# Performance work log

Hardware: AMD Instinct MI355X
Metric: run time of the kernel (lower is better)

The kernel has to match this reference:

```python
import jax, jax.numpy as jnp
import numpy as np

D_MODEL = 1024
HEADS = 16
HEAD_DIM = D_MODEL // HEADS


def setup_inputs() -> dict:
    key = jax.random.key(0)
    ks = jax.random.split(key, 6)
    B, S, D = 2, 2048, D_MODEL
    scale = 1.0 / np.sqrt(D)
    x = jax.random.normal(ks[0], (B, S, D), dtype=jnp.float32)
    mask = jax.random.randint(ks[1], (B, S), 0, 2, dtype=jnp.int32)
    Wq = jax.random.normal(ks[2], (D, D), dtype=jnp.float32) * scale
    Wk = jax.random.normal(ks[3], (D, D), dtype=jnp.float32) * scale
    Wv = jax.random.normal(ks[4], (D, D), dtype=jnp.float32) * scale
    Wp = jax.random.normal(ks[5], (D, D), dtype=jnp.float32) * scale
    zb = jnp.zeros((D,), dtype=jnp.float32)
    return {"x": x, "mask": mask, "Wq": Wq, "bq": zb, "Wk": Wk, "bk": zb,
            "Wv": Wv, "bv": zb, "Wp": Wp, "bp": zb}


def reference(x, mask, Wq, bq, Wk, bk, Wv, bv, Wp, bp):
    B, S, D = x.shape
    H, Dh = HEADS, HEAD_DIM

    def split_heads(t):  # [B,S,D] -> [B,H,S,Dh]
        return t.reshape(B, S, H, Dh).transpose(0, 2, 1, 3)

    q = split_heads(x @ Wq + bq)
    k = split_heads(x @ Wk + bk)
    v = split_heads(x @ Wv + bv)

    att = jnp.einsum('bhqd,bhkd->bhqk', q, k) / jnp.sqrt(jnp.float32(Dh))
    # key-padding mask: [B,S] -> [B,1,1,S]; masked positions -> -inf
    m = (mask[:, None, None, :] != 0)
    att = jnp.where(m, att, -jnp.inf)
    att = jax.nn.softmax(att, axis=-1)
    # rows that were fully masked produce NaN -> zero them (masked_fill(isnan, 0))
    att = jnp.where(jnp.isnan(att), 0.0, att)

    y = jnp.einsum('bhqk,bhkd->bhqd', att, v)  # [B,H,S,Dh]
    y = y.transpose(0, 2, 1, 3).reshape(B, S, D)
    return y @ Wp + bp
```

## Files before the change

### kernel.cpp

```cpp
#include <hip/hip_runtime.h>
#include <math.h>

#define D_MODEL 1024
#define HEADS 16
#define HEAD_DIM 64
#define SEQ 2048
#define BATCH 2
#define KVT 64
#define QTILE 64

typedef __attribute__((ext_vector_type(8))) short bf16x8;
typedef __attribute__((ext_vector_type(4))) float f32x4;

__device__ __forceinline__ short f2bf(float f) {
    union { float f; unsigned u; } v; v.f = f;
    unsigned r = (v.u + 0x7FFFu + ((v.u >> 16) & 1u)) >> 16;
    return (short)r;
}

__device__ __forceinline__ unsigned cvt_pk_bf16(float lo, float hi) {
    unsigned r;
    asm("v_cvt_pk_bf16_f32 %0, %1, %2" : "=v"(r) : "v"(lo), "v"(hi));
    return r;
}

__global__ __launch_bounds__(256) void convert_bf16(
    const float* __restrict__ in, short* __restrict__ out, int n8) {
    int i = blockIdx.x * 256 + threadIdx.x;
    if (i >= n8) return;
    float4 a = ((const float4*)in)[2 * i];
    float4 b = ((const float4*)in)[2 * i + 1];
    short r[8] = {f2bf(a.x), f2bf(a.y), f2bf(a.z), f2bf(a.w),
                  f2bf(b.x), f2bf(b.y), f2bf(b.z), f2bf(b.w)};
    *(uint4*)(out + 8 * i) = *(uint4*)r;
}

__global__ __launch_bounds__(256) void mask_to_float(
    const int* __restrict__ mask, float* __restrict__ mf, int n) {
    int i = blockIdx.x * 256 + threadIdx.x;
    if (i < n) mf[i] = mask[i] ? 0.f : -INFINITY;
}

__global__ __launch_bounds__(256) void wtrans(
    const float* __restrict__ Wq, const float* __restrict__ Wk,
    const float* __restrict__ Wv, const float* __restrict__ Wp,
    short* __restrict__ Wqkvt, short* __restrict__ Wpt) {
    __shared__ float t[32][33];
    const int z = blockIdx.z;
    const float* W = z == 0 ? Wq : z == 1 ? Wk : z == 2 ? Wv : Wp;
    short* dst = (z < 3) ? Wqkvt + (size_t)z * 1024 * 1024 : Wpt;
    const int n0 = blockIdx.x * 32, k0 = blockIdx.y * 32;
    const int tx = threadIdx.x & 31, ty = threadIdx.x >> 5;
#pragma unroll
    for (int j = 0; j < 4; ++j)
        t[ty + j * 8][tx] = W[(size_t)(k0 + ty + j * 8) * 1024 + n0 + tx];
    __syncthreads();
#pragma unroll
    for (int j = 0; j < 4; ++j) {
        const int n = ty + j * 8;
        dst[(size_t)(n0 + n) * 1024 + k0 + tx] = f2bf(t[tx][n]);
    }
}

template <int MODE>
__global__ __launch_bounds__(256) void mfma_gemm(
    const short* __restrict__ A, const short* __restrict__ Bt,
    const float* __restrict__ b0, const float* __restrict__ b1,
    const float* __restrict__ b2, float* __restrict__ outf,
    short* __restrict__ o0, short* __restrict__ o1, short* __restrict__ o2,
    int M, int N, int K) {
    __shared__ short As[2 * 128 * 32];
    __shared__ short Bs[2 * 128 * 32];

    const int tid = threadIdx.x;
    const int wave = tid >> 6, lane = tid & 63;
    const int l15 = lane & 15, lhi = lane >> 4;
    const int wm = wave >> 1, wn = wave & 1;
    const int bm0 = blockIdx.y * 128, bn0 = blockIdx.x * 128;

    f32x4 acc[4][4];
#pragma unroll
    for (int m = 0; m < 4; ++m)
#pragma unroll
        for (int n = 0; n < 4; ++n) acc[m][n] = (f32x4){0.f, 0.f, 0.f, 0.f};

#define STAGE_G(buf, kt_)                                                         \
    {                                                                             \
        const int k0 = (kt_) * 32;                                                \
        _Pragma("unroll") for (int p = 0; p < 2; ++p) {                           \
            const int o = (wave * 2 + p) * 64 + lane;                             \
            const int r = o >> 2;                                                 \
            const int gs = (o & 3) ^ ((r >> 1) & 3);                              \
            __builtin_amdgcn_global_load_lds(                                     \
                (const __attribute__((address_space(1))) void*)(                  \
                    A + (size_t)(bm0 + r) * K + k0 + gs * 8),                     \
                (__attribute__((address_space(3))) void*)(                        \
                    As + (size_t)(buf) * 4096 + (wave * 2 + p) * 512),            \
                16, 0, 0);                                                        \
            __builtin_amdgcn_global_load_lds(                                     \
                (const __attribute__((address_space(1))) void*)(                  \
                    Bt + (size_t)(bn0 + r) * K + k0 + gs * 8),                    \
                (__attribute__((address_space(3))) void*)(                        \
                    Bs + (size_t)(buf) * 4096 + (wave * 2 + p) * 512),            \
                16, 0, 0);                                                        \
        }                                                                         \
    }

    const int NT = K / 32;
    STAGE_G(0, 0);
    __syncthreads();
    for (int kt = 0; kt < NT; ++kt) {
        const int cur = kt & 1;
        if (kt + 1 < NT) STAGE_G((kt + 1) & 1, kt + 1);
        bf16x8 af[4], bf[4];
        const int sg = (lhi ^ ((l15 >> 1) & 3)) * 16;
#pragma unroll
        for (int m = 0; m < 4; ++m)
            af[m] = *(const bf16x8*)((char*)As + cur * 8192 +
                                     (wm * 64 + m * 16 + l15) * 64 + sg);
#pragma unroll
        for (int n = 0; n < 4; ++n)
            bf[n] = *(const bf16x8*)((char*)Bs + cur * 8192 +
                                     (wn * 64 + n * 16 + l15) * 64 + sg);
        __builtin_amdgcn_s_setprio(1);
#pragma unroll
        for (int m = 0; m < 4; ++m)
#pragma unroll
            for (int n = 0; n < 4; ++n)
                acc[m][n] = __builtin_amdgcn_mfma_f32_16x16x32_bf16(af[m], bf[n], acc[m][n], 0, 0, 0);
        __builtin_amdgcn_s_setprio(0);
        __syncthreads();
    }
#undef STAGE_G

#pragma unroll
    for (int m = 0; m < 4; ++m) {
#pragma unroll
        for (int n = 0; n < 4; ++n) {
            const int col = bn0 + wn * 64 + n * 16 + l15;
#pragma unroll
            for (int rr = 0; rr < 4; ++rr) {
                const int row = bm0 + wm * 64 + m * 16 + lhi * 4 + rr;
                const float v = acc[m][n][rr];
                if (MODE == 0) {
                    outf[(size_t)row * N + col] = v + b0[col];
                } else {
                    const int which = col >> 10;
                    const int cc = col & 1023;
                    const int h = cc >> 6, dh = cc & 63;
                    const int b = row >> 11, s = row & (SEQ - 1);
                    const float bias = (which == 0 ? b0 : which == 1 ? b1 : b2)[cc];
                    short* dst = which == 0 ? o0 : which == 1 ? o1 : o2;
                    dst[(((size_t)(b * HEADS + h)) * SEQ + s) * HEAD_DIM + dh] = f2bf(v + bias);
                }
            }
        }
    }
}

__global__ __launch_bounds__(256) void transpose_v(
    const short* __restrict__ V, short* __restrict__ Vt) {
    __shared__ short t[64][66];
    const int bh = blockIdx.y, s0 = blockIdx.x * 64;
    const int tx = threadIdx.x, ty = threadIdx.y;
    const short* src = V + ((size_t)bh * SEQ + s0) * 64;
#pragma unroll
    for (int j = 0; j < 16; ++j) {
        const int sl = ty * 16 + j;
        t[sl][tx] = src[(size_t)sl * 64 + tx];
    }
    __syncthreads();
    short* dst = Vt + (size_t)bh * 64 * SEQ + s0;
#pragma unroll
    for (int j = 0; j < 16; ++j) {
        const int dh = ty * 16 + j;
        dst[(size_t)dh * SEQ + tx] = t[tx][dh];
    }
}

__global__ __launch_bounds__(256, 4) void flash_attn(
    const short* __restrict__ Q, const short* __restrict__ K,
    const short* __restrict__ Vt, const float* __restrict__ maskf,
    short* __restrict__ Y) {
    __shared__ unsigned char kt[2][KVT * 128];
    __shared__ unsigned char vt[2][HEAD_DIM * 128];
    __shared__ unsigned char pb[4][16 * 128];

    const int tid = threadIdx.x;
    const int wave = tid >> 6;
    const int lane = tid & 63;
    const int l15 = lane & 15;
    const int lhi = lane >> 4;

    const int nwg = gridDim.x;
    const int wg = blockIdx.x;
    const int swz = (wg & 7) * (nwg >> 3) + (wg >> 3);
    const int qt = swz & 31;
    const int bh = swz >> 5;
    const int b = bh >> 4;

    const int q0 = qt * QTILE + wave * 16;

    const short* Qp = Q + ((size_t)bh * SEQ + q0 + l15) * HEAD_DIM;
    bf16x8 qf[2];
    qf[0] = *(const bf16x8*)(Qp + 8 * lhi);
    qf[1] = *(const bf16x8*)(Qp + 8 * lhi + 32);

    const unsigned char* Kb8 = (const unsigned char*)(K + (size_t)bh * SEQ * HEAD_DIM);
    const unsigned char* Vb8 = (const unsigned char*)(Vt + (size_t)bh * HEAD_DIM * SEQ);
    const float* mb = maskf + b * SEQ;

#define STAGE(buf, kvi)                                                            \
    {                                                                              \
        const unsigned char* kbase = Kb8 + (size_t)(kvi) * KVT * 128;              \
        const unsigned char* vbase = Vb8 + (size_t)(kvi) * 128;                    \
        _Pragma("unroll") for (int p = 0; p < 2; ++p) {                            \
            const int o = (wave * 2 + p) * 64 + lane;                              \
            const int row = o >> 3;                                                \
            const int inner = (o & 7) * 16;                                        \
            const int src = inner ^ ((row & 7) << 4);                              \
            __builtin_amdgcn_global_load_lds(                                      \
                (const __attribute__((address_space(1))) void*)(                   \
                    kbase + row * 128 + src),                                      \
                (__attribute__((address_space(3))) void*)(                         \
                    &kt[buf][(wave * 2 + p) * 1024]),                              \
                16, 0, 0);                                                         \
            __builtin_amdgcn_global_load_lds(                                      \
                (const __attribute__((address_space(1))) void*)(                   \
                    vbase + (size_t)row * (SEQ * 2) + src),                        \
                (__attribute__((address_space(3))) void*)(                         \
                    &vt[buf][(wave * 2 + p) * 1024]),                              \
                16, 0, 0);                                                         \
        }                                                                          \
    }

    f32x4 accO[4];
    float mrow = -30000.f, lrow = 0.f;
#pragma unroll
    for (int i = 0; i < 4; ++i) accO[i] = (f32x4){0.f, 0.f, 0.f, 0.f};

    STAGE(0, 0);
    __syncthreads();

    for (int kv = 0; kv < SEQ / KVT; ++kv) {
        const int cur = kv & 1;
        if (kv + 1 < SEQ / KVT) STAGE((kv + 1) & 1, kv + 1);

        const int k0 = kv * KVT;

        f32x4 accS[4];
#pragma unroll
        for (int nt = 0; nt < 4; ++nt) accS[nt] = (f32x4){0.f, 0.f, 0.f, 0.f};
#pragma unroll
        for (int c = 0; c < 2; ++c) {
            bf16x8 kf[4];
#pragma unroll
            for (int nt = 0; nt < 4; ++nt) {
                const int key = l15 + 16 * nt;
                kf[nt] = *(const bf16x8*)(kt[cur] + key * 128 +
                                          ((16 * lhi + 64 * c) ^ ((key & 7) << 4)));
            }
            __builtin_amdgcn_s_setprio(1);
#pragma unroll
            for (int nt = 0; nt < 4; ++nt)
                accS[nt] = __builtin_amdgcn_mfma_f32_16x16x32_bf16(kf[nt], qf[c], accS[nt], 0, 0, 0);
            __builtin_amdgcn_s_setprio(0);
        }

#pragma unroll
        for (int nt = 0; nt < 4; ++nt) {
            const f32x4 ma = *(const f32x4*)(mb + k0 + 16 * nt + 4 * lhi);
#pragma unroll
            for (int r = 0; r < 4; ++r) accS[nt][r] = accS[nt][r] * 0.125f + ma[r];
        }

        float smax = accS[0][0];
#pragma unroll
        for (int nt = 0; nt < 4; ++nt)
#pragma unroll
            for (int r = 0; r < 4; ++r) smax = fmaxf(smax, accS[nt][r]);
        smax = fmaxf(smax, __shfl_xor(smax, 16));
        smax = fmaxf(smax, __shfl_xor(smax, 32));

        if (!__all(smax <= mrow + 8.f)) {
            const float mn = fmaxf(mrow, smax);
            const float alpha = __expf(mrow - mn);
            lrow *= alpha;
#pragma unroll
            for (int d = 0; d < 4; ++d)
#pragma unroll
                for (int r = 0; r < 4; ++r) accO[d][r] *= alpha;
            mrow = mn;
        }

        float rs = 0.f;
#pragma unroll
        for (int nt = 0; nt < 4; ++nt)
#pragma unroll
            for (int r = 0; r < 4; ++r) {
                const float pv = __expf(accS[nt][r] - mrow);
                accS[nt][r] = pv;
                rs += pv;
            }
        rs += __shfl_xor(rs, 16);
        rs += __shfl_xor(rs, 32);
        lrow += rs;

#pragma unroll
        for (int nt = 0; nt < 4; ++nt) {
            uint2 w;
            w.x = cvt_pk_bf16(accS[nt][0], accS[nt][1]);
            w.y = cvt_pk_bf16(accS[nt][2], accS[nt][3]);
            *(uint2*)(pb[wave] + l15 * 128 +
                      ((32 * nt + 8 * lhi) ^ ((l15 & 7) << 4))) = w;
        }

#pragma unroll
        for (int c = 0; c < 2; ++c) {
            bf16x8 pf = *(const bf16x8*)(pb[wave] + l15 * 128 +
                                         ((16 * lhi + 64 * c) ^ ((l15 & 7) << 4)));
            bf16x8 vf[4];
#pragma unroll
            for (int d = 0; d < 4; ++d) {
                const int dh = l15 + 16 * d;
                vf[d] = *(const bf16x8*)(vt[cur] + dh * 128 +
                                         ((16 * lhi + 64 * c) ^ ((dh & 7) << 4)));
            }
            __builtin_amdgcn_s_setprio(1);
#pragma unroll
            for (int d = 0; d < 4; ++d)
                accO[d] = __builtin_amdgcn_mfma_f32_16x16x32_bf16(vf[d], pf, accO[d], 0, 0, 0);
            __builtin_amdgcn_s_setprio(0);
        }
        __syncthreads();
    }
#undef STAGE

    const float inv = (lrow > 0.f) ? 1.f / lrow : 0.f;
    const int qg = q0 + l15;
    short* Yp = Y + ((size_t)b * SEQ + qg) * D_MODEL + (bh & 15) * HEAD_DIM;
#pragma unroll
    for (int d = 0; d < 4; ++d) {
        uint2 w;
        w.x = cvt_pk_bf16(accO[d][0] * inv, accO[d][1] * inv);
        w.y = cvt_pk_bf16(accO[d][2] * inv, accO[d][3] * inv);
        *(uint2*)(Yp + 16 * d + 4 * lhi) = w;
    }
}

extern "C" void kernel_launch(void* const* d_in, const int* in_sizes, int n_in,
                              void* d_out, int out_size, void* d_ws, size_t ws_size,
                              hipStream_t stream) {
    const float* x    = (const float*)d_in[0];
    const int*   mask = (const int*)  d_in[1];
    const float* Wq   = (const float*)d_in[2];
    const float* bq   = (const float*)d_in[3];
    const float* Wk   = (const float*)d_in[4];
    const float* bk   = (const float*)d_in[5];
    const float* Wv   = (const float*)d_in[6];
    const float* bv   = (const float*)d_in[7];
    const float* Wp   = (const float*)d_in[8];
    const float* bp   = (const float*)d_in[9];
    float* out = (float*)d_out;

    short* ws    = (short*)d_ws;
    short* xb    = ws;
    short* Wqkvt = xb + ((size_t)4 << 20);
    short* Wpt   = Wqkvt + ((size_t)3 << 20);
    short* Qb    = Wpt + ((size_t)1 << 20);
    short* Kb    = Qb + ((size_t)4 << 20);
    short* Vb    = Kb + ((size_t)4 << 20);
    short* Vtb   = Vb + ((size_t)4 << 20);
    short* Yb    = Vtb + ((size_t)4 << 20);
    float* maskf = (float*)Vb;

    const int M = BATCH * SEQ;

    convert_bf16<<<dim3((M * D_MODEL / 8 + 255) / 256), 256, 0, stream>>>(x, xb, M * D_MODEL / 8);
    wtrans<<<dim3(32, 32, 4), 256, 0, stream>>>(Wq, Wk, Wv, Wp, Wqkvt, Wpt);

    mfma_gemm<1><<<dim3(3 * D_MODEL / 128, M / 128), 256, 0, stream>>>(
        xb, Wqkvt, bq, bk, bv, nullptr, Qb, Kb, Vb, M, 3 * D_MODEL, D_MODEL);

    transpose_v<<<dim3(SEQ / 64, BATCH * HEADS), dim3(64, 4), 0, stream>>>(Vb, Vtb);

    mask_to_float<<<dim3((BATCH * SEQ + 255) / 256), 256, 0, stream>>>(mask, maskf, BATCH * SEQ);

    flash_attn<<<dim3(BATCH * HEADS * (SEQ / QTILE)), 256, 0, stream>>>(Qb, Kb, Vtb, maskf, Yb);

    mfma_gemm<0><<<dim3(D_MODEL / 128, M / 128), 256, 0, stream>>>(
        Yb, Wpt, bp, bp, bp, out, nullptr, nullptr, nullptr, M, D_MODEL, D_MODEL);
}
```

Baseline: 144.0 us.

## Fuse prep kernels, write V transposed from GEMM, fold softmax scale into Q

Merges the x conversion, weight transposes and mask conversion into one prep launch. The QKV GEMM epilogue now writes V directly in transposed layout with packed stores, which removes the separate transpose_v kernel and its buffer. Q is pre-scaled by log2(e)/sqrt(Dh), so attention uses the raw v_exp_f32 (exp2) and drops the per-score multiply. The rescale threshold is widened to match the base-2 domain, the P buffer swizzle changes, and P is read as two 8-byte LDS loads. The scale is applied before the bf16 rounding of Q, so numerics shift slightly.

```diff
diff --git a/kernel.cpp b/kernel.cpp
--- a/kernel.cpp
+++ b/kernel.cpp
@@ -8,6 +8,7 @@
 #define BATCH 2
 #define KVT 64
 #define QTILE 64
+#define SCALE_Q 0.18033688f
 
 typedef __attribute__((ext_vector_type(8))) short bf16x8;
 typedef __attribute__((ext_vector_type(4))) float f32x4;
@@ -24,41 +25,47 @@
     return r;
 }
 
-__global__ __launch_bounds__(256) void convert_bf16(
-    const float* __restrict__ in, short* __restrict__ out, int n8) {
-    int i = blockIdx.x * 256 + threadIdx.x;
-    if (i >= n8) return;
-    float4 a = ((const float4*)in)[2 * i];
-    float4 b = ((const float4*)in)[2 * i + 1];
-    short r[8] = {f2bf(a.x), f2bf(a.y), f2bf(a.z), f2bf(a.w),
-                  f2bf(b.x), f2bf(b.y), f2bf(b.z), f2bf(b.w)};
-    *(uint4*)(out + 8 * i) = *(uint4*)r;
-}
-
-__global__ __launch_bounds__(256) void mask_to_float(
-    const int* __restrict__ mask, float* __restrict__ mf, int n) {
-    int i = blockIdx.x * 256 + threadIdx.x;
-    if (i < n) mf[i] = mask[i] ? 0.f : -INFINITY;
-}
-
-__global__ __launch_bounds__(256) void wtrans(
-    const float* __restrict__ Wq, const float* __restrict__ Wk,
-    const float* __restrict__ Wv, const float* __restrict__ Wp,
-    short* __restrict__ Wqkvt, short* __restrict__ Wpt) {
+__device__ __forceinline__ float fexp2(float x) {
+    float r;
+    asm("v_exp_f32 %0, %1" : "=v"(r) : "v"(x));
+    return r;
+}
+
+__global__ __launch_bounds__(256) void prep(
+    const float* __restrict__ x, const float* __restrict__ Wq,
+    const float* __restrict__ Wk, const float* __restrict__ Wv,
+    const float* __restrict__ Wp, const int* __restrict__ mask,
+    short* __restrict__ xb, short* __restrict__ Wqkvt,
+    short* __restrict__ Wpt, float* __restrict__ maskf) {
     __shared__ float t[32][33];
-    const int z = blockIdx.z;
-    const float* W = z == 0 ? Wq : z == 1 ? Wk : z == 2 ? Wv : Wp;
-    short* dst = (z < 3) ? Wqkvt + (size_t)z * 1024 * 1024 : Wpt;
-    const int n0 = blockIdx.x * 32, k0 = blockIdx.y * 32;
-    const int tx = threadIdx.x & 31, ty = threadIdx.x >> 5;
-#pragma unroll
-    for (int j = 0; j < 4; ++j)
-        t[ty + j * 8][tx] = W[(size_t)(k0 + ty + j * 8) * 1024 + n0 + tx];
-    __syncthreads();
-#pragma unroll
-    for (int j = 0; j < 4; ++j) {
-        const int n = ty + j * 8;
-        dst[(size_t)(n0 + n) * 1024 + k0 + tx] = f2bf(t[tx][n]);
+    const int bid = blockIdx.x;
+    if (bid < 2048) {
+        const int i = bid * 256 + threadIdx.x;
+        float4 a = ((const float4*)x)[2 * i];
+        float4 b = ((const float4*)x)[2 * i + 1];
+        short r[8] = {f2bf(a.x), f2bf(a.y), f2bf(a.z), f2bf(a.w),
+                      f2bf(b.x), f2bf(b.y), f2bf(b.z), f2bf(b.w)};
+        *(uint4*)(xb + 8 * i) = *(uint4*)r;
+    } else if (bid < 6144) {
+        const int tt = bid - 2048;
+        const int z = tt >> 10;
+        const int rem = tt & 1023;
+        const float* W = z == 0 ? Wq : z == 1 ? Wk : z == 2 ? Wv : Wp;
+        short* dst = (z < 3) ? Wqkvt + (size_t)z * 1024 * 1024 : Wpt;
+        const int n0 = (rem & 31) * 32, k0 = (rem >> 5) * 32;
+        const int tx = threadIdx.x & 31, ty = threadIdx.x >> 5;
+#pragma unroll
+        for (int j = 0; j < 4; ++j)
+            t[ty + j * 8][tx] = W[(size_t)(k0 + ty + j * 8) * 1024 + n0 + tx];
+        __syncthreads();
+#pragma unroll
+        for (int j = 0; j < 4; ++j) {
+            const int n = ty + j * 8;
+            dst[(size_t)(n0 + n) * 1024 + k0 + tx] = f2bf(t[tx][n]);
+        }
+    } else {
+        const int i = (bid - 6144) * 256 + threadIdx.x;
+        maskf[i] = mask[i] ? 0.f : -INFINITY;
     }
 }
 
@@ -133,48 +140,41 @@
     }
 #undef STAGE_G
 
+    const int which = (MODE == 1) ? (bn0 >> 10) : 0;
 #pragma unroll
     for (int m = 0; m < 4; ++m) {
 #pragma unroll
         for (int n = 0; n < 4; ++n) {
             const int col = bn0 + wn * 64 + n * 16 + l15;
-#pragma unroll
-            for (int rr = 0; rr < 4; ++rr) {
-                const int row = bm0 + wm * 64 + m * 16 + lhi * 4 + rr;
-                const float v = acc[m][n][rr];
-                if (MODE == 0) {
-                    outf[(size_t)row * N + col] = v + b0[col];
+            if (MODE == 0) {
+#pragma unroll
+                for (int rr = 0; rr < 4; ++rr) {
+                    const int row = bm0 + wm * 64 + m * 16 + lhi * 4 + rr;
+                    outf[(size_t)row * N + col] = acc[m][n][rr] + b0[col];
+                }
+            } else {
+                const int cc = col & 1023;
+                const int h = cc >> 6, dh = cc & 63;
+                const int row0 = bm0 + wm * 64 + m * 16 + lhi * 4;
+                const int b = row0 >> 11, s0 = row0 & (SEQ - 1);
+                if (which == 2) {
+                    const float bias = b2[cc];
+                    uint2 w;
+                    w.x = cvt_pk_bf16(acc[m][n][0] + bias, acc[m][n][1] + bias);
+                    w.y = cvt_pk_bf16(acc[m][n][2] + bias, acc[m][n][3] + bias);
+                    *(uint2*)(o2 + ((size_t)(b * HEADS + h) * HEAD_DIM + dh) * SEQ + s0) = w;
                 } else {
-                    const int which = col >> 10;
-                    const int cc = col & 1023;
-                    const int h = cc >> 6, dh = cc & 63;
-                    const int b = row >> 11, s = row & (SEQ - 1);
-                    const float bias = (which == 0 ? b0 : which == 1 ? b1 : b2)[cc];
-                    short* dst = which == 0 ? o0 : which == 1 ? o1 : o2;
-                    dst[(((size_t)(b * HEADS + h)) * SEQ + s) * HEAD_DIM + dh] = f2bf(v + bias);
+                    const float bias = (which == 0 ? b0 : b1)[cc];
+                    short* dst = which == 0 ? o0 : o1;
+#pragma unroll
+                    for (int rr = 0; rr < 4; ++rr) {
+                        float v = acc[m][n][rr] + bias;
+                        if (which == 0) v *= SCALE_Q;
+                        dst[(((size_t)(b * HEADS + h)) * SEQ + s0 + rr) * HEAD_DIM + dh] = f2bf(v);
+                    }
                 }
             }
         }
-    }
-}
-
-__global__ __launch_bounds__(256) void transpose_v(
-    const short* __restrict__ V, short* __restrict__ Vt) {
-    __shared__ short t[64][66];
-    const int bh = blockIdx.y, s0 = blockIdx.x * 64;
-    const int tx = threadIdx.x, ty = threadIdx.y;
-    const short* src = V + ((size_t)bh * SEQ + s0) * 64;
-#pragma unroll
-    for (int j = 0; j < 16; ++j) {
-        const int sl = ty * 16 + j;
-        t[sl][tx] = src[(size_t)sl * 64 + tx];
-    }
-    __syncthreads();
-    short* dst = Vt + (size_t)bh * 64 * SEQ + s0;
-#pragma unroll
-    for (int j = 0; j < 16; ++j) {
-        const int dh = ty * 16 + j;
-        dst[(size_t)dh * SEQ + tx] = t[tx][dh];
     }
 }
 
@@ -271,20 +271,20 @@
         for (int nt = 0; nt < 4; ++nt) {
             const f32x4 ma = *(const f32x4*)(mb + k0 + 16 * nt + 4 * lhi);
 #pragma unroll
-            for (int r = 0; r < 4; ++r) accS[nt][r] = accS[nt][r] * 0.125f + ma[r];
-        }
-
-        float smax = accS[0][0];
-#pragma unroll
-        for (int nt = 0; nt < 4; ++nt)
-#pragma unroll
-            for (int r = 0; r < 4; ++r) smax = fmaxf(smax, accS[nt][r]);
+            for (int r = 0; r < 4; ++r) accS[nt][r] += ma[r];
+        }
+
+        float t0 = fmaxf(fmaxf(accS[0][0], accS[0][1]), fmaxf(accS[0][2], accS[0][3]));
+        float t1 = fmaxf(fmaxf(accS[1][0], accS[1][1]), fmaxf(accS[1][2], accS[1][3]));
+        float t2 = fmaxf(fmaxf(accS[2][0], accS[2][1]), fmaxf(accS[2][2], accS[2][3]));
+        float t3 = fmaxf(fmaxf(accS[3][0], accS[3][1]), fmaxf(accS[3][2], accS[3][3]));
+        float smax = fmaxf(fmaxf(t0, t1), fmaxf(t2, t3));
         smax = fmaxf(smax, __shfl_xor(smax, 16));
         smax = fmaxf(smax, __shfl_xor(smax, 32));
 
-        if (!__all(smax <= mrow + 8.f)) {
+        if (!__all(smax <= mrow + 11.5f)) {
             const float mn = fmaxf(mrow, smax);
-            const float alpha = __expf(mrow - mn);
+            const float alpha = fexp2(mrow - mn);
             lrow *= alpha;
 #pragma unroll
             for (int d = 0; d < 4; ++d)
@@ -298,7 +298,7 @@
         for (int nt = 0; nt < 4; ++nt)
 #pragma unroll
             for (int r = 0; r < 4; ++r) {
-                const float pv = __expf(accS[nt][r] - mrow);
+                const float pv = fexp2(accS[nt][r] - mrow);
                 accS[nt][r] = pv;
                 rs += pv;
             }
@@ -311,14 +311,17 @@
             uint2 w;
             w.x = cvt_pk_bf16(accS[nt][0], accS[nt][1]);
             w.y = cvt_pk_bf16(accS[nt][2], accS[nt][3]);
-            *(uint2*)(pb[wave] + l15 * 128 +
-                      ((32 * nt + 8 * lhi) ^ ((l15 & 7) << 4))) = w;
+            *(uint2*)(pb[wave] + l15 * 128 + ((32 * nt + 8 * lhi) ^ (l15 << 3))) = w;
         }
 
 #pragma unroll
         for (int c = 0; c < 2; ++c) {
-            bf16x8 pf = *(const bf16x8*)(pb[wave] + l15 * 128 +
-                                         ((16 * lhi + 64 * c) ^ ((l15 & 7) << 4)));
+            union { bf16x8 v; uint2 u[2]; } pfu;
+            pfu.u[0] = *(const uint2*)(pb[wave] + l15 * 128 +
+                                       ((16 * lhi + 64 * c) ^ (l15 << 3)));
+            pfu.u[1] = *(const uint2*)(pb[wave] + l15 * 128 +
+                                       ((16 * lhi + 64 * c + 8) ^ (l15 << 3)));
+            const bf16x8 pf = pfu.v;
             bf16x8 vf[4];
 #pragma unroll
             for (int d = 0; d < 4; ++d) {
@@ -369,22 +372,17 @@
     short* Wpt   = Wqkvt + ((size_t)3 << 20);
     short* Qb    = Wpt + ((size_t)1 << 20);
     short* Kb    = Qb + ((size_t)4 << 20);
-    short* Vb    = Kb + ((size_t)4 << 20);
-    short* Vtb   = Vb + ((size_t)4 << 20);
+    short* Vtb   = Kb + ((size_t)4 << 20);
     short* Yb    = Vtb + ((size_t)4 << 20);
-    float* maskf = (float*)Vb;
+    float* maskf = (float*)(Yb + ((size_t)4 << 20));
 
     const int M = BATCH * SEQ;
 
-    convert_bf16<<<dim3((M * D_MODEL / 8 + 255) / 256), 256, 0, stream>>>(x, xb, M * D_MODEL / 8);
-    wtrans<<<dim3(32, 32, 4), 256, 0, stream>>>(Wq, Wk, Wv, Wp, Wqkvt, Wpt);
+    prep<<<dim3(6160), 256, 0, stream>>>(x, Wq, Wk, Wv, Wp, mask,
+                                         xb, Wqkvt, Wpt, maskf);
 
     mfma_gemm<1><<<dim3(3 * D_MODEL / 128, M / 128), 256, 0, stream>>>(
-        xb, Wqkvt, bq, bk, bv, nullptr, Qb, Kb, Vb, M, 3 * D_MODEL, D_MODEL);
-
-    transpose_v<<<dim3(SEQ / 64, BATCH * HEADS), dim3(64, 4), 0, stream>>>(Vb, Vtb);
-
-    mask_to_float<<<dim3((BATCH * SEQ + 255) / 256), 256, 0, stream>>>(mask, maskf, BATCH * SEQ);
+        xb, Wqkvt, bq, bk, bv, nullptr, Qb, Kb, Vtb, M, 3 * D_MODEL, D_MODEL);
 
     flash_attn<<<dim3(BATCH * HEADS * (SEQ / QTILE)), 256, 0, stream>>>(Qb, Kb, Vtb, maskf, Yb);
 
```

Result: faster. 135.2 us (-6.2%).
